# Performance work log

Hardware: AMD Instinct MI355X
Metric: run time of the kernel (lower is better)

## Reference

```python
import jax, jax.numpy as jnp
import numpy as np

# Complete 32-ary tree of depth 3: vocab = 32**3 = 32768 leaves.
B = 4096       # batch
NHID = 512     # hidden size
BR = 32        # branching factor (num_children at every internal node)
DEPTH = 3      # number of internal-node decisions from root to leaf
V = BR ** DEPTH
NUM_NODES = sum(BR ** k for k in range(DEPTH))  # 1 + 32 + 1024 = 1057

# Static tree-indexing tables (level-order node numbering).
_LEVEL_OFFSET = np.array([sum(BR ** j for j in range(k)) for k in range(DEPTH)], dtype=np.int64)   # [0, 1, 33]
_NODE_DIV = np.array([BR ** (DEPTH - k) for k in range(DEPTH)], dtype=np.int64)                    # node-within-level divisor
_STEP_DIV = np.array([BR ** (DEPTH - 1 - k) for k in range(DEPTH)], dtype=np.int64)                # child-step divisor


def setup_inputs() -> dict:
    key = jax.random.key(0)
    k1, k2, k3 = jax.random.split(key, 3)
    inputs = jax.random.normal(k1, (B, NHID), dtype=jnp.float32)
    labels = jax.random.randint(k2, (B,), 0, V)                     # leaf index per sample
    W = jax.random.normal(k3, (NUM_NODES, NHID, BR), dtype=jnp.float32)  # all node params, stacked
    return {"inputs": inputs, "labels": labels, "W": W}


def reference(inputs, labels, W):
    lab = labels[:, None]                                            # [B, 1]
    node_idx = jnp.asarray(_LEVEL_OFFSET)[None, :] + lab // jnp.asarray(_NODE_DIV)[None, :]  # [B, D] node on path
    steps = (lab // jnp.asarray(_STEP_DIV)[None, :]) % BR            # [B, D] child taken at each node
    Wg = W[node_idx]                                                 # [B, D, NHID, BR] gathered path params
    logits = jnp.einsum('bh,bdhc->bdc', inputs, Wg)                  # [B, D, BR]
    p = jax.nn.softmax(logits, axis=-1)
    step_p = jnp.take_along_axis(p, steps[:, :, None], axis=-1)[..., 0]  # [B, D]
    return jnp.prod(step_p, axis=-1)                                 # [B] path probability
```

## Files before the change

### kernel.cpp

```cpp
#include <hip/hip_runtime.h>


#define NHID   512
#define BR     32
#define BATCH  4096
#define NBUCK  1024
#define SMAX   8
#define CAP    64
#define CROWS  32
#define CFLT   (CROWS * BR)
#define NCHUNK (NHID / CROWS)

#define FMA4(A, xv, wv_) do { \
    (A).x = fmaf((xv), (wv_).x, (A).x); \
    (A).y = fmaf((xv), (wv_).y, (A).y); \
    (A).z = fmaf((xv), (wv_).z, (A).z); \
    (A).w = fmaf((xv), (wv_).w, (A).w); } while (0)

__device__ __forceinline__ void gload_lds16(const float* g, float* l) {
    __builtin_amdgcn_global_load_lds(
        (const __attribute__((address_space(1))) void*)g,
        (__attribute__((address_space(3))) void*)l, 16, 0, 0);
}

__global__ __launch_bounds__(192) void hsm_bucket(
    const float* __restrict__ inputs,
    const int* __restrict__ labels,
    const float* __restrict__ W,
    float* __restrict__ out)
{
    __shared__ float xsT[NHID * SMAX];
    __shared__ float wb[3][2][CFLT];
    __shared__ float pk[3][SMAX];
    __shared__ int   sids[CAP];
    __shared__ int   slab[CAP];
    __shared__ int   scnt;

    const int g    = blockIdx.x;
    const int tid  = threadIdx.x;
    const int k    = tid >> 6;
    const int lane = tid & 63;
    const int colg = lane & 7;
    const int hsel = lane >> 3;

    const int node   = (k == 0) ? 0 : (k == 1) ? 1 + (g >> 5) : 33 + g;
    const int step01 = (k == 0) ? (g >> 5) : (g & 31);

    const float* wglob  = W + (size_t)node * (NHID * BR) + lane * 4;
    float* const wbase0 = wb[k][0];
    float* const wbase1 = wb[k][1];

    #define ISSUE(c, bptr) do { \
        const float* gs_ = wglob + (size_t)(c) * CFLT; \
        gload_lds16(gs_,       (bptr)); \
        gload_lds16(gs_ + 256, (bptr) + 256); \
        gload_lds16(gs_ + 512, (bptr) + 512); \
        gload_lds16(gs_ + 768, (bptr) + 768); } while (0)

    ISSUE(0, wbase0);
    ISSUE(1, wbase1);

    if (tid == 0) scnt = 0;
    __syncthreads();

    const int4* l4 = (const int4*)labels;
    for (int i = tid; i < BATCH / 4; i += 192) {
        const int4 v = l4[i];
        if ((v.x >> 5) == g) { int p = atomicAdd(&scnt, 1); if (p < CAP) { sids[p] = 4*i;   slab[p] = v.x; } }
        if ((v.y >> 5) == g) { int p = atomicAdd(&scnt, 1); if (p < CAP) { sids[p] = 4*i+1; slab[p] = v.y; } }
        if ((v.z >> 5) == g) { int p = atomicAdd(&scnt, 1); if (p < CAP) { sids[p] = 4*i+2; slab[p] = v.z; } }
        if ((v.w >> 5) == g) { int p = atomicAdd(&scnt, 1); if (p < CAP) { sids[p] = 4*i+3; slab[p] = v.w; } }
    }
    __syncthreads();
    const int mt = min(scnt, CAP);
    if (mt == 0) {
        asm volatile("s_waitcnt vmcnt(0)" ::: "memory");
        return;
    }

    const float4* xf = (const float4*)xsT;

    for (int c0 = 0; c0 < mt; c0 += SMAX) {
        if (c0 > 0) {
            ISSUE(0, wbase0);
            ISSUE(1, wbase1);
        }

        for (int h = tid; h < NHID; h += 192) {
            float v[SMAX];
            #pragma unroll
            for (int s = 0; s < SMAX; ++s) {
                const int q = c0 + s;
                v[s] = (q < mt) ? inputs[(size_t)sids[q] * NHID + h] : 0.0f;
            }
            float4* dst = (float4*)&xsT[h * SMAX];
            dst[0] = make_float4(v[0], v[1], v[2], v[3]);
            dst[1] = make_float4(v[4], v[5], v[6], v[7]);
        }
        __syncthreads();

        float4 acc[SMAX];
        #pragma unroll
        for (int s = 0; s < SMAX; ++s) acc[s] = make_float4(0, 0, 0, 0);

        #pragma unroll
        for (int c = 0; c < NCHUNK; ++c) {
            if (c < NCHUNK - 1) asm volatile("s_waitcnt vmcnt(4)" ::: "memory");
            else                asm volatile("s_waitcnt vmcnt(0)" ::: "memory");
            __builtin_amdgcn_sched_barrier(0);
            const float4* wf = (const float4*)((c & 1) ? wbase1 : wbase0);
            #pragma unroll
            for (int j = 0; j < 4; ++j) {
                const int r = hsel + 8 * j;
                const float4 wv = wf[r * 8 + colg];
                const float4 xa = xf[(c * CROWS + r) * 2];
                const float4 xb = xf[(c * CROWS + r) * 2 + 1];
                FMA4(acc[0], xa.x, wv); FMA4(acc[1], xa.y, wv);
                FMA4(acc[2], xa.z, wv); FMA4(acc[3], xa.w, wv);
                FMA4(acc[4], xb.x, wv); FMA4(acc[5], xb.y, wv);
                FMA4(acc[6], xb.z, wv); FMA4(acc[7], xb.w, wv);
            }
            if (c + 2 < NCHUNK) ISSUE(c + 2, (c & 1) ? wbase1 : wbase0);
        }

        #pragma unroll
        for (int s = 0; s < SMAX; ++s) {
            #pragma unroll
            for (int mm = 8; mm <= 32; mm <<= 1) {
                acc[s].x += __shfl_xor(acc[s].x, mm);
                acc[s].y += __shfl_xor(acc[s].y, mm);
                acc[s].z += __shfl_xor(acc[s].z, mm);
                acc[s].w += __shfl_xor(acc[s].w, mm);
            }
        }

        #pragma unroll
        for (int s = 0; s < SMAX; ++s) {
            float4 a = acc[s];
            float mx = fmaxf(fmaxf(a.x, a.y), fmaxf(a.z, a.w));
            #pragma unroll
            for (int mm = 1; mm <= 4; mm <<= 1) mx = fmaxf(mx, __shfl_xor(mx, mm));
            float es = expf(a.x - mx) + expf(a.y - mx) + expf(a.z - mx) + expf(a.w - mx);
            #pragma unroll
            for (int mm = 1; mm <= 4; mm <<= 1) es += __shfl_xor(es, mm);

            const int step = (k == 2) ? (slab[c0 + s] & 31) : step01;
            const int e = step & 3;
            const float vv = (e == 0) ? a.x : (e == 1) ? a.y : (e == 2) ? a.z : a.w;
            const float sl = __shfl(vv, step >> 2);
            const float p = expf(sl - mx) / es;
            if (lane == 0) pk[k][s] = p;
        }
        __syncthreads();

        if (tid < SMAX && c0 + tid < mt)
            out[sids[c0 + tid]] = pk[0][tid] * pk[1][tid] * pk[2][tid];
    }
    #undef ISSUE
}

extern "C" void kernel_launch(void* const* d_in, const int* in_sizes, int n_in,
                              void* d_out, int out_size, void* d_ws, size_t ws_size,
                              hipStream_t stream)
{
    const float* inputs = (const float*)d_in[0];
    const int*   labels = (const int*)d_in[1];
    const float* W      = (const float*)d_in[2];
    float* out = (float*)d_out;

    hsm_bucket<<<dim3(NBUCK), dim3(192), 0, stream>>>(inputs, labels, W, out);
}
```

Before: 150.9 us.

## Triple-buffer weight chunks and batch LDS reads via inline asm

```diff
diff --git a/kernel.cpp b/kernel.cpp
--- a/kernel.cpp
+++ b/kernel.cpp
@@ -10,6 +10,7 @@
 #define CROWS  32
 #define CFLT   (CROWS * BR)
 #define NCHUNK (NHID / CROWS)
+#define NBUF   3
 
 #define FMA4(A, xv, wv_) do { \
     (A).x = fmaf((xv), (wv_).x, (A).x); \
@@ -23,6 +24,16 @@
         (__attribute__((address_space(3))) void*)l, 16, 0, 0);
 }
 
+__device__ __forceinline__ uint32_t lds_a(const void* p) {
+    return (uint32_t)(uintptr_t)(const __attribute__((address_space(3))) void*)p;
+}
+
+__device__ __forceinline__ float4 dsr128(uint32_t a) {
+    float4 r;
+    asm volatile("ds_read_b128 %0, %1" : "=v"(r) : "v"(a));
+    return r;
+}
+
 __global__ __launch_bounds__(192) void hsm_bucket(
     const float* __restrict__ inputs,
     const int* __restrict__ labels,
@@ -30,7 +41,7 @@
     float* __restrict__ out)
 {
     __shared__ float xsT[NHID * SMAX];
-    __shared__ float wb[3][2][CFLT];
+    __shared__ float wb[3][NBUF][CFLT];
     __shared__ float pk[3][SMAX];
     __shared__ int   sids[CAP];
     __shared__ int   slab[CAP];
@@ -46,19 +57,15 @@
     const int node   = (k == 0) ? 0 : (k == 1) ? 1 + (g >> 5) : 33 + g;
     const int step01 = (k == 0) ? (g >> 5) : (g & 31);
 
-    const float* wglob  = W + (size_t)node * (NHID * BR) + lane * 4;
-    float* const wbase0 = wb[k][0];
-    float* const wbase1 = wb[k][1];
+    const float* wglob = W + (size_t)node * (NHID * BR) + lane * 4;
 
-    #define ISSUE(c, bptr) do { \
+    #define ISSUE(c, b) do { \
         const float* gs_ = wglob + (size_t)(c) * CFLT; \
-        gload_lds16(gs_,       (bptr)); \
-        gload_lds16(gs_ + 256, (bptr) + 256); \
-        gload_lds16(gs_ + 512, (bptr) + 512); \
-        gload_lds16(gs_ + 768, (bptr) + 768); } while (0)
-
-    ISSUE(0, wbase0);
-    ISSUE(1, wbase1);
+        float* ld_ = wb[k][(b)]; \
+        gload_lds16(gs_,       ld_); \
+        gload_lds16(gs_ + 256, ld_ + 256); \
+        gload_lds16(gs_ + 512, ld_ + 512); \
+        gload_lds16(gs_ + 768, ld_ + 768); } while (0)
 
     if (tid == 0) scnt = 0;
     __syncthreads();
@@ -73,18 +80,15 @@
     }
     __syncthreads();
     const int mt = min(scnt, CAP);
-    if (mt == 0) {
-        asm volatile("s_waitcnt vmcnt(0)" ::: "memory");
-        return;
-    }
+    if (mt == 0) return;
 
-    const float4* xf = (const float4*)xsT;
+    const uint32_t wA0 = lds_a(&wb[k][0][0]) + (uint32_t)lane * 16;
+    const uint32_t wA1 = lds_a(&wb[k][1][0]) + (uint32_t)lane * 16;
+    const uint32_t wA2 = lds_a(&wb[k][2][0]) + (uint32_t)lane * 16;
+    const uint32_t xA  = lds_a(xsT) + (uint32_t)hsel * 32;
 
     for (int c0 = 0; c0 < mt; c0 += SMAX) {
-        if (c0 > 0) {
-            ISSUE(0, wbase0);
-            ISSUE(1, wbase1);
-        }
+        if (c0 > 0) __syncthreads();
 
         for (int h = tid; h < NHID; h += 192) {
             float v[SMAX];
@@ -99,28 +103,42 @@
         }
         __syncthreads();
 
+        ISSUE(0, 0); ISSUE(1, 1); ISSUE(2, 2);
+
         float4 acc[SMAX];
         #pragma unroll
         for (int s = 0; s < SMAX; ++s) acc[s] = make_float4(0, 0, 0, 0);
 
         #pragma unroll
         for (int c = 0; c < NCHUNK; ++c) {
-            if (c < NCHUNK - 1) asm volatile("s_waitcnt vmcnt(4)" ::: "memory");
-            else                asm volatile("s_waitcnt vmcnt(0)" ::: "memory");
+            if (c == NCHUNK - 1)      asm volatile("s_waitcnt vmcnt(0)" ::: "memory");
+            else if (c == NCHUNK - 2) asm volatile("s_waitcnt vmcnt(4)" ::: "memory");
+            else                      asm volatile("s_waitcnt vmcnt(8)" ::: "memory");
             __builtin_amdgcn_sched_barrier(0);
-            const float4* wf = (const float4*)((c & 1) ? wbase1 : wbase0);
+
+            const uint32_t wbase = (c % NBUF == 0) ? wA0 : (c % NBUF == 1) ? wA1 : wA2;
+            const uint32_t xbase = xA + (uint32_t)(c * CROWS) * 32;
+
+            float4 wv[4], xa[4], xb[4];
             #pragma unroll
             for (int j = 0; j < 4; ++j) {
-                const int r = hsel + 8 * j;
-                const float4 wv = wf[r * 8 + colg];
-                const float4 xa = xf[(c * CROWS + r) * 2];
-                const float4 xb = xf[(c * CROWS + r) * 2 + 1];
-                FMA4(acc[0], xa.x, wv); FMA4(acc[1], xa.y, wv);
-                FMA4(acc[2], xa.z, wv); FMA4(acc[3], xa.w, wv);
-                FMA4(acc[4], xb.x, wv); FMA4(acc[5], xb.y, wv);
-                FMA4(acc[6], xb.z, wv); FMA4(acc[7], xb.w, wv);
+                wv[j] = dsr128(wbase + (uint32_t)j * 1024);
+                xa[j] = dsr128(xbase + (uint32_t)j * 256);
+                xb[j] = dsr128(xbase + (uint32_t)j * 256 + 16);
             }
-            if (c + 2 < NCHUNK) ISSUE(c + 2, (c & 1) ? wbase1 : wbase0);
+            asm volatile("s_waitcnt lgkmcnt(0)" ::: "memory");
+            __builtin_amdgcn_sched_barrier(0);
+
+            if (c + NBUF < NCHUNK) ISSUE(c + NBUF, c % NBUF);
+            __builtin_amdgcn_sched_barrier(0);
+
+            #pragma unroll
+            for (int j = 0; j < 4; ++j) {
+                FMA4(acc[0], xa[j].x, wv[j]); FMA4(acc[1], xa[j].y, wv[j]);
+                FMA4(acc[2], xa[j].z, wv[j]); FMA4(acc[3], xa[j].w, wv[j]);
+                FMA4(acc[4], xb[j].x, wv[j]); FMA4(acc[5], xb[j].y, wv[j]);
+                FMA4(acc[6], xb[j].z, wv[j]); FMA4(acc[7], xb[j].w, wv[j]);
+            }
         }
 
         #pragma unroll
```

Measured after the change: 183.2 us. 21.4% more time.
